# Kernel tuning notes

Measured on AMD Instinct MI355X. Metric: run time of the kernel, lower is better.

## Reference

```python
import jax, jax.numpy as jnp
import numpy as np

N, D, H = 8192, 64, 128
GRID = 256
RADIUS2 = 9  # radius=3 squared


def setup_inputs() -> dict:
    key = jax.random.key(0)
    ks = jax.random.split(key, 9)
    s = lambda k, shape, scale: jax.random.normal(k, shape, dtype=jnp.float32) * scale
    return {
        "positions": jax.random.randint(ks[0], (N, 2), 0, GRID, dtype=jnp.int32),
        "states": s(ks[1], (N, D), 0.1),
        "h": s(ks[2], (N, H), 0.1),
        "c": s(ks[3], (N, H), 0.1),
        "W_ih": s(ks[4], (4 * H, 2 * D), 1.0 / np.sqrt(2 * D)),
        "W_hh": s(ks[5], (4 * H, H), 1.0 / np.sqrt(H)),
        "b": s(ks[6], (4 * H,), 0.01),
        "W_out": s(ks[7], (H, D), 1.0 / np.sqrt(H)),
        "W_role": s(ks[8], (H, 3), 1.0 / np.sqrt(H)),
    }


def reference(positions, states, h, c, W_ih, W_hh, b, W_out, W_role):
    # --- neighbor gather: all-pairs distance on integer grid, radius 3 ---
    d = positions[:, None, :] - positions[None, :, :]          # [N,N,2]
    dist2 = jnp.sum(d * d, axis=-1)                            # [N,N] int32
    mask = (dist2 <= RADIUS2) & (~jnp.eye(N, dtype=bool))      # exclude self
    maskf = mask.astype(states.dtype)
    cnt = jnp.sum(maskf, axis=1, keepdims=True)                # [N,1]
    # mean of neighbor states; zeros when no neighbors (matches zeros fallback)
    nbr_mean = (maskf @ states) / jnp.maximum(cnt, 1.0)        # [N,D]

    # --- per-cell LSTM memory update ---
    x = jnp.concatenate([states, nbr_mean], axis=-1)           # [N,2D]
    gates = x @ W_ih.T + h @ W_hh.T + b                        # [N,4H]
    i_g, f_g, g_g, o_g = jnp.split(gates, 4, axis=-1)
    c_new = jax.nn.sigmoid(f_g) * c + jax.nn.sigmoid(i_g) * jnp.tanh(g_g)
    h_new = jax.nn.sigmoid(o_g) * jnp.tanh(c_new)              # [N,H]

    new_states = h_new @ W_out                                 # [N,D]
    role_probs = jax.nn.softmax(h_new @ W_role, axis=-1)       # [N,3]
    return new_states, role_probs
```

## Files before the change

### kernel.cpp

```cpp
#include <hip/hip_runtime.h>
#include <hip/hip_bf16.h>
#include <math.h>

#define N_CELLS 8192
#define D_DIM 64
#define H_DIM 128
#define GRID_SZ 256
#define NBINS (GRID_SZ * GRID_SZ)
#define BUCKET_CAP 16

typedef short bf16x8 __attribute__((ext_vector_type(8)));
typedef float f32x4 __attribute__((ext_vector_type(4)));

static __device__ __forceinline__ short f2bf(float x) {
    __hip_bfloat16 b = __float2bfloat16(x);
    return __builtin_bit_cast(short, b);
}

__global__ __launch_bounds__(256) void prep(const float* __restrict__ Wih,
                                            const float* __restrict__ Whh,
                                            __hip_bfloat16* __restrict__ Wb,
                                            int4* __restrict__ counts4) {
    int tid = threadIdx.x, b = blockIdx.x;
    if (b >= 128) {
        counts4[(b - 128) * 256 + tid] = make_int4(0, 0, 0, 0);
        return;
    }
    int idx4 = b * 256 + tid;
    int gp = idx4 >> 6, k4 = (idx4 & 63) << 2;
    int group = gp >> 6, c6 = gp & 63, gate = c6 >> 4, hl = c6 & 15;
    int orig = gate * 128 + group * 16 + hl;
    float4 v = (k4 < 128) ? *(const float4*)(Wih + orig * 128 + k4)
                          : *(const float4*)(Whh + orig * 128 + (k4 - 128));
    short4 o = make_short4(f2bf(v.x), f2bf(v.y), f2bf(v.z), f2bf(v.w));
    *(short4*)((short*)Wb + gp * 256 + k4) = o;
}

__global__ __launch_bounds__(256) void bin_fill(const int* __restrict__ positions,
                                                int* __restrict__ counts,
                                                int* __restrict__ buckets) {
    int i = blockIdx.x * 256 + threadIdx.x;
    if (i >= N_CELLS) return;
    int p0 = positions[2 * i], p1 = positions[2 * i + 1];
    int bin = p0 * GRID_SZ + p1;
    int slot = atomicAdd(&counts[bin], 1);
    if (slot < BUCKET_CAP) buckets[bin * BUCKET_CAP + slot] = i;
}

__global__ __launch_bounds__(256) void build_xh(const int* __restrict__ positions,
                                                const float* __restrict__ states,
                                                const float* __restrict__ h,
                                                const int* __restrict__ counts,
                                                const int* __restrict__ buckets,
                                                __hip_bfloat16* __restrict__ xh) {
    int wave = threadIdx.x >> 6;
    int lane = threadIdx.x & 63;
    int i = blockIdx.x * 4 + wave;
    int p0 = positions[2 * i], p1 = positions[2 * i + 1];

    int t = lane;
    int da, db;
    if (t == 0)      { da = -3; db = 0; }
    else if (t < 6)  { da = -2; db = t - 3; }
    else if (t < 11) { da = -1; db = t - 8; }
    else if (t < 18) { da = 0;  db = t - 14; }
    else if (t < 23) { da = 1;  db = t - 20; }
    else if (t < 28) { da = 2;  db = t - 25; }
    else             { da = 3;  db = 0; }

    int q0 = p0 + da, q1 = p1 + db;
    bool ok = (lane < 29) && ((unsigned)q0 < GRID_SZ) && ((unsigned)q1 < GRID_SZ);
    int bin = q0 * GRID_SZ + q1;

    int cl = 0;
    int4 jv = make_int4(0, 0, 0, 0);
    if (ok) {
        cl = counts[bin];
        jv = *(const int4*)(buckets + bin * BUCKET_CAP);
        if (cl > BUCKET_CAP) cl = BUCKET_CAP;
    }

    unsigned long long act = __ballot(cl > 0);
    float acc = 0.0f;
    int cnt = 0;
    while (act) {
        int tb = __ffsll(act) - 1;
        act &= act - 1;
        int ct = __shfl(cl, tb);
        int j0 = __shfl(jv.x, tb), j1 = __shfl(jv.y, tb);
        int j2 = __shfl(jv.z, tb), j3 = __shfl(jv.w, tb);
        if (j0 != i)           { cnt++; acc += states[j0 * D_DIM + lane]; }
        if (ct > 1 && j1 != i) { cnt++; acc += states[j1 * D_DIM + lane]; }
        if (ct > 2 && j2 != i) { cnt++; acc += states[j2 * D_DIM + lane]; }
        if (ct > 3 && j3 != i) { cnt++; acc += states[j3 * D_DIM + lane]; }
        if (ct > 4) {
            int bb = __shfl(bin, tb) * BUCKET_CAP;
            for (int s = 4; s < ct; ++s) {
                int j = buckets[bb + s];
                if (j != i) { cnt++; acc += states[j * D_DIM + lane]; }
            }
        }
    }
    float nbr = (cnt > 0) ? acc / (float)cnt : 0.0f;

    __hip_bfloat16* row = xh + (size_t)i * 256;
    row[lane]       = __float2bfloat16(states[i * D_DIM + lane]);
    row[64 + lane]  = __float2bfloat16(nbr);
    row[128 + lane] = __float2bfloat16(h[i * H_DIM + lane]);
    row[192 + lane] = __float2bfloat16(h[i * H_DIM + 64 + lane]);
}

__global__ __launch_bounds__(512) void mega(const __hip_bfloat16* __restrict__ xh,
                                            const __hip_bfloat16* __restrict__ Wb,
                                            const float* __restrict__ bias,
                                            const float* __restrict__ c_in,
                                            const float* __restrict__ W_out,
                                            const float* __restrict__ W_role,
                                            float* __restrict__ out) {
    __shared__ char smem[69632];
    char* As = smem;
    char* Bs = smem + 4096;
    char* Hl   = smem;
    char* Wohi = smem + 8192;
    char* Wolo = smem + 24576;
    char* Wr   = smem + 40960;

    const int tid  = threadIdx.x;
    const int lane = tid & 63;
    const int wid  = tid >> 6;
    const int wrow = wid >> 2, wcol = wid & 3;
    const int n0 = blockIdx.x * 32;

    const char* aG = (const char*)xh;
    const char* bG = (const char*)Wb;

    f32x4 acc[8] = {};

    for (int kc = 0; kc < 4; ++kc) {
        if (kc) __syncthreads();
        if (tid < 256) {
            int row = tid >> 3, slot = (tid & 7) << 4;
            __builtin_amdgcn_global_load_lds(
                (const __attribute__((address_space(1))) void*)(aG + (size_t)(n0 + row) * 512 + kc * 128 + (slot ^ ((row & 7) << 4))),
                (__attribute__((address_space(3))) void*)(As + row * 128 + slot), 16, 0, 0);
        }
        #pragma unroll
        for (int e = 0; e < 8; ++e) {
            int u = e * 512 + tid;
            int row = u >> 3, slot = (u & 7) << 4;
            __builtin_amdgcn_global_load_lds(
                (const __attribute__((address_space(1))) void*)(bG + (size_t)row * 512 + kc * 128 + (slot ^ ((row & 7) << 4))),
                (__attribute__((address_space(3))) void*)(Bs + row * 128 + slot), 16, 0, 0);
        }
        __syncthreads();

        #pragma unroll
        for (int ks = 0; ks < 2; ++ks) {
            int kb = ks * 64 + ((lane >> 4) << 4);
            int arow = wrow * 16 + (lane & 15);
            bf16x8 av = *(const bf16x8*)(As + arow * 128 + (kb ^ ((arow & 7) << 4)));
            #pragma unroll
            for (int ni = 0; ni < 8; ++ni) {
                int brow = wcol * 128 + ni * 16 + (lane & 15);
                bf16x8 bv = *(const bf16x8*)(Bs + brow * 128 + (kb ^ ((brow & 7) << 4)));
                acc[ni] = __builtin_amdgcn_mfma_f32_16x16x32_bf16(av, bv, acc[ni], 0, 0, 0);
            }
        }
    }
    __syncthreads();

    #pragma unroll
    for (int e = 0; e < 16; ++e) {
        int u = e * 512 + tid;
        int hh = u >> 6, d = u & 63;
        float w = W_out[u];
        float whi = __bfloat162float(__float2bfloat16(w));
        int off = d * 256 + ((hh * 2) ^ ((d & 7) << 4));
        *(short*)(Wohi + off) = f2bf(whi);
        *(short*)(Wolo + off) = f2bf(w - whi);
    }
    #pragma unroll
    for (int e = 0; e < 4; ++e) {
        int u = e * 512 + tid;
        int r = u >> 7, hh = u & 127;
        float w = (r < 3) ? W_role[hh * 3 + r] : 0.0f;
        *(short*)(Wr + r * 256 + ((hh * 2) ^ ((r & 7) << 4))) = f2bf(w);
    }

    #pragma unroll
    for (int b = 0; b < 2; ++b) {
        int hg = (2 * wcol + b) * 16 + (lane & 15);
        float bi = bias[hg], bff = bias[128 + hg], bgg = bias[256 + hg], boo = bias[384 + hg];
        #pragma unroll
        for (int r = 0; r < 4; ++r) {
            int ml = wrow * 16 + ((lane >> 4) << 2) + r;
            float ig = acc[b * 4 + 0][r] + bi;
            float fg = acc[b * 4 + 1][r] + bff;
            float gg = acc[b * 4 + 2][r] + bgg;
            float og = acc[b * 4 + 3][r] + boo;
            float cv = c_in[(size_t)(n0 + ml) * H_DIM + hg];
            float si = 1.0f / (1.0f + expf(-ig));
            float sf = 1.0f / (1.0f + expf(-fg));
            float so = 1.0f / (1.0f + expf(-og));
            float hn = so * tanhf(sf * cv + si * tanhf(gg));
            *(short*)(Hl + ml * 256 + ((hg * 2) ^ ((ml & 7) << 4))) = f2bf(hn);
        }
    }
    __syncthreads();

    const int rb = wid >> 2, db = wid & 3;
    f32x4 oacc = {};
    f32x4 racc = {};
    #pragma unroll
    for (int ks = 0; ks < 4; ++ks) {
        int kb = ks * 64 + ((lane >> 4) << 4);
        int hrow = rb * 16 + (lane & 15);
        bf16x8 hv = *(const bf16x8*)(Hl + hrow * 256 + (kb ^ ((hrow & 7) << 4)));
        int drow = db * 16 + (lane & 15);
        int woff = drow * 256 + (kb ^ ((drow & 7) << 4));
        bf16x8 whi = *(const bf16x8*)(Wohi + woff);
        bf16x8 wlo = *(const bf16x8*)(Wolo + woff);
        oacc = __builtin_amdgcn_mfma_f32_16x16x32_bf16(hv, whi, oacc, 0, 0, 0);
        oacc = __builtin_amdgcn_mfma_f32_16x16x32_bf16(hv, wlo, oacc, 0, 0, 0);
        if (db == 3) {
            int rrow = lane & 15;
            bf16x8 wr = *(const bf16x8*)(Wr + rrow * 256 + (kb ^ ((rrow & 7) << 4)));
            racc = __builtin_amdgcn_mfma_f32_16x16x32_bf16(wr, hv, racc, 0, 0, 0);
        }
    }
    #pragma unroll
    for (int r = 0; r < 4; ++r) {
        int m = n0 + rb * 16 + ((lane >> 4) << 2) + r;
        out[(size_t)m * D_DIM + db * 16 + (lane & 15)] = oacc[r];
    }
    if (db == 3 && lane < 16) {
        int m = n0 + rb * 16 + lane;
        float l0 = racc[0], l1 = racc[1], l2 = racc[2];
        float mx = fmaxf(l0, fmaxf(l1, l2));
        float e0 = expf(l0 - mx), e1 = expf(l1 - mx), e2 = expf(l2 - mx);
        float s = e0 + e1 + e2;
        float* ro = out + (size_t)N_CELLS * D_DIM + (size_t)m * 3;
        ro[0] = e0 / s; ro[1] = e1 / s; ro[2] = e2 / s;
    }
}

extern "C" void kernel_launch(void* const* d_in, const int* in_sizes, int n_in,
                              void* d_out, int out_size, void* d_ws, size_t ws_size,
                              hipStream_t stream) {
    const int*   positions = (const int*)d_in[0];
    const float* states    = (const float*)d_in[1];
    const float* h         = (const float*)d_in[2];
    const float* c         = (const float*)d_in[3];
    const float* Wih       = (const float*)d_in[4];
    const float* Whh       = (const float*)d_in[5];
    const float* bias      = (const float*)d_in[6];
    const float* Wout      = (const float*)d_in[7];
    const float* Wrole     = (const float*)d_in[8];
    float* out             = (float*)d_out;

    char* ws = (char*)d_ws;
    int*            counts  = (int*)ws;
    int*            buckets = (int*)(ws + 262144);
    __hip_bfloat16* xh      = (__hip_bfloat16*)(ws + 4456448);
    __hip_bfloat16* Wb      = (__hip_bfloat16*)(ws + 8650752);

    prep<<<192, 256, 0, stream>>>(Wih, Whh, Wb, (int4*)counts);
    bin_fill<<<N_CELLS / 256, 256, 0, stream>>>(positions, counts, buckets);
    build_xh<<<N_CELLS / 4, 256, 0, stream>>>(positions, states, h, counts, buckets, xh);
    mega<<<N_CELLS / 32, 512, 0, stream>>>(xh, Wb, bias, c, Wout, Wrole, out);
}
```

Before: 34.59 us.

## Precompute output/role weight bf16 splits in prep and async-load them into LDS

Moves the W_out hi/lo bf16 split and the W_role conversion out of each mega block and into the prep kernel, which writes them to workspace. Mega then loads them into dedicated LDS regions with async global_load_lds at the start, overlapping that load with the gate GEMM. It also prefetches the c values into registers before the GEMM. The cost is LDS growing from 68KB to 112KB per block, which may limit occupancy, plus a larger prep launch.

Measured after the change: 33.61 us. -2.8%, faster.

```diff
diff --git a/kernel.cpp b/kernel.cpp
--- a/kernel.cpp
+++ b/kernel.cpp
@@ -19,21 +19,41 @@
 
 __global__ __launch_bounds__(256) void prep(const float* __restrict__ Wih,
                                             const float* __restrict__ Whh,
+                                            const float* __restrict__ W_out,
+                                            const float* __restrict__ W_role,
                                             __hip_bfloat16* __restrict__ Wb,
+                                            __hip_bfloat16* __restrict__ Wohi,
+                                            __hip_bfloat16* __restrict__ Wolo,
+                                            __hip_bfloat16* __restrict__ Wr,
                                             int4* __restrict__ counts4) {
     int tid = threadIdx.x, b = blockIdx.x;
-    if (b >= 128) {
+    if (b < 128) {
+        int idx4 = b * 256 + tid;
+        int gp = idx4 >> 6, k4 = (idx4 & 63) << 2;
+        int group = gp >> 6, c6 = gp & 63, gate = c6 >> 4, hl = c6 & 15;
+        int orig = gate * 128 + group * 16 + hl;
+        float4 v = (k4 < 128) ? *(const float4*)(Wih + orig * 128 + k4)
+                              : *(const float4*)(Whh + orig * 128 + (k4 - 128));
+        short4 o = make_short4(f2bf(v.x), f2bf(v.y), f2bf(v.z), f2bf(v.w));
+        *(short4*)((short*)Wb + gp * 256 + k4) = o;
+    } else if (b < 192) {
         counts4[(b - 128) * 256 + tid] = make_int4(0, 0, 0, 0);
-        return;
-    }
-    int idx4 = b * 256 + tid;
-    int gp = idx4 >> 6, k4 = (idx4 & 63) << 2;
-    int group = gp >> 6, c6 = gp & 63, gate = c6 >> 4, hl = c6 & 15;
-    int orig = gate * 128 + group * 16 + hl;
-    float4 v = (k4 < 128) ? *(const float4*)(Wih + orig * 128 + k4)
-                          : *(const float4*)(Whh + orig * 128 + (k4 - 128));
-    short4 o = make_short4(f2bf(v.x), f2bf(v.y), f2bf(v.z), f2bf(v.w));
-    *(short4*)((short*)Wb + gp * 256 + k4) = o;
+    } else if (b < 224) {
+        int u = (b - 192) * 256 + tid;
+        int hh = u >> 6, d = u & 63;
+        float w = W_out[u];
+        float whi = __bfloat162float(__float2bfloat16(w));
+        Wohi[d * 128 + hh] = __float2bfloat16(whi);
+        Wolo[d * 128 + hh] = __float2bfloat16(w - whi);
+    } else {
+        #pragma unroll
+        for (int e = 0; e < 8; ++e) {
+            int u = e * 256 + tid;
+            int r = u >> 7, hh = u & 127;
+            float w = (r < 3) ? W_role[hh * 3 + r] : 0.0f;
+            Wr[r * 128 + hh] = __float2bfloat16(w);
+        }
+    }
 }
 
 __global__ __launch_bounds__(256) void bin_fill(const int* __restrict__ positions,
@@ -114,22 +134,56 @@
                                             const __hip_bfloat16* __restrict__ Wb,
                                             const float* __restrict__ bias,
                                             const float* __restrict__ c_in,
-                                            const float* __restrict__ W_out,
-                                            const float* __restrict__ W_role,
+                                            const __hip_bfloat16* __restrict__ Wohi,
+                                            const __hip_bfloat16* __restrict__ Wolo,
+                                            const __hip_bfloat16* __restrict__ Wr,
                                             float* __restrict__ out) {
-    __shared__ char smem[69632];
-    char* As = smem;
-    char* Bs = smem + 4096;
-    char* Hl   = smem;
-    char* Wohi = smem + 8192;
-    char* Wolo = smem + 24576;
-    char* Wr   = smem + 40960;
+    __shared__ char smem[114688];
+    char* As  = smem;
+    char* Bs  = smem + 4096;
+    char* Whi = smem + 69632;
+    char* Wlo = smem + 86016;
+    char* Wrl = smem + 102400;
+    char* Hl  = smem + 106496;
 
     const int tid  = threadIdx.x;
     const int lane = tid & 63;
     const int wid  = tid >> 6;
     const int wrow = wid >> 2, wcol = wid & 3;
     const int n0 = blockIdx.x * 32;
+
+    const char* hiG = (const char*)Wohi;
+    const char* loG = (const char*)Wolo;
+    const char* wrG = (const char*)Wr;
+    #pragma unroll
+    for (int e = 0; e < 2; ++e) {
+        int u = e * 512 + tid;
+        int row = u >> 4, slot = (u & 15) << 4;
+        int src = row * 256 + (slot ^ ((row & 7) << 4));
+        __builtin_amdgcn_global_load_lds(
+            (const __attribute__((address_space(1))) void*)(hiG + src),
+            (__attribute__((address_space(3))) void*)(Whi + row * 256 + slot), 16, 0, 0);
+        __builtin_amdgcn_global_load_lds(
+            (const __attribute__((address_space(1))) void*)(loG + src),
+            (__attribute__((address_space(3))) void*)(Wlo + row * 256 + slot), 16, 0, 0);
+    }
+    if (tid < 256) {
+        int row = tid >> 4, slot = (tid & 15) << 4;
+        __builtin_amdgcn_global_load_lds(
+            (const __attribute__((address_space(1))) void*)(wrG + row * 256 + (slot ^ ((row & 7) << 4))),
+            (__attribute__((address_space(3))) void*)(Wrl + row * 256 + slot), 16, 0, 0);
+    }
+
+    float cv[2][4];
+    #pragma unroll
+    for (int b = 0; b < 2; ++b) {
+        int hg = (2 * wcol + b) * 16 + (lane & 15);
+        #pragma unroll
+        for (int r = 0; r < 4; ++r) {
+            int ml = wrow * 16 + ((lane >> 4) << 2) + r;
+            cv[b][r] = c_in[(size_t)(n0 + ml) * H_DIM + hg];
+        }
+    }
 
     const char* aG = (const char*)xh;
     const char* bG = (const char*)Wb;
@@ -167,25 +221,6 @@
             }
         }
     }
-    __syncthreads();
-
-    #pragma unroll
-    for (int e = 0; e < 16; ++e) {
-        int u = e * 512 + tid;
-        int hh = u >> 6, d = u & 63;
-        float w = W_out[u];
-        float whi = __bfloat162float(__float2bfloat16(w));
-        int off = d * 256 + ((hh * 2) ^ ((d & 7) << 4));
-        *(short*)(Wohi + off) = f2bf(whi);
-        *(short*)(Wolo + off) = f2bf(w - whi);
-    }
-    #pragma unroll
-    for (int e = 0; e < 4; ++e) {
-        int u = e * 512 + tid;
-        int r = u >> 7, hh = u & 127;
-        float w = (r < 3) ? W_role[hh * 3 + r] : 0.0f;
-        *(short*)(Wr + r * 256 + ((hh * 2) ^ ((r & 7) << 4))) = f2bf(w);
-    }
 
     #pragma unroll
     for (int b = 0; b < 2; ++b) {
@@ -198,11 +233,10 @@
             float fg = acc[b * 4 + 1][r] + bff;
             float gg = acc[b * 4 + 2][r] + bgg;
             float og = acc[b * 4 + 3][r] + boo;
-            float cv = c_in[(size_t)(n0 + ml) * H_DIM + hg];
             float si = 1.0f / (1.0f + expf(-ig));
             float sf = 1.0f / (1.0f + expf(-fg));
             float so = 1.0f / (1.0f + expf(-og));
-            float hn = so * tanhf(sf * cv + si * tanhf(gg));
+            float hn = so * tanhf(sf * cv[b][r] + si * tanhf(gg));
             *(short*)(Hl + ml * 256 + ((hg * 2) ^ ((ml & 7) << 4))) = f2bf(hn);
         }
     }
@@ -218,13 +252,13 @@
         bf16x8 hv = *(const bf16x8*)(Hl + hrow * 256 + (kb ^ ((hrow & 7) << 4)));
         int drow = db * 16 + (lane & 15);
         int woff = drow * 256 + (kb ^ ((drow & 7) << 4));
-        bf16x8 whi = *(const bf16x8*)(Wohi + woff);
-        bf16x8 wlo = *(const bf16x8*)(Wolo + woff);
+        bf16x8 whi = *(const bf16x8*)(Whi + woff);
+        bf16x8 wlo = *(const bf16x8*)(Wlo + woff);
         oacc = __builtin_amdgcn_mfma_f32_16x16x32_bf16(hv, whi, oacc, 0, 0, 0);
         oacc = __builtin_amdgcn_mfma_f32_16x16x32_bf16(hv, wlo, oacc, 0, 0, 0);
         if (db == 3) {
             int rrow = lane & 15;
-            bf16x8 wr = *(const bf16x8*)(Wr + rrow * 256 + (kb ^ ((rrow & 7) << 4)));
+            bf16x8 wr = *(const bf16x8*)(Wrl + rrow * 256 + (kb ^ ((rrow & 7) << 4)));
             racc = __builtin_amdgcn_mfma_f32_16x16x32_bf16(wr, hv, racc, 0, 0, 0);
         }
     }
@@ -263,9 +297,12 @@
     int*            buckets = (int*)(ws + 262144);
     __hip_bfloat16* xh      = (__hip_bfloat16*)(ws + 4456448);
     __hip_bfloat16* Wb      = (__hip_bfloat16*)(ws + 8650752);
-
-    prep<<<192, 256, 0, stream>>>(Wih, Whh, Wb, (int4*)counts);
+    __hip_bfloat16* Wohi    = (__hip_bfloat16*)(ws + 8912896);
+    __hip_bfloat16* Wolo    = (__hip_bfloat16*)(ws + 8929280);
+    __hip_bfloat16* Wr      = (__hip_bfloat16*)(ws + 8945664);
+
+    prep<<<225, 256, 0, stream>>>(Wih, Whh, Wout, Wrole, Wb, Wohi, Wolo, Wr, (int4*)counts);
     bin_fill<<<N_CELLS / 256, 256, 0, stream>>>(positions, counts, buckets);
     build_xh<<<N_CELLS / 4, 256, 0, stream>>>(positions, states, h, counts, buckets, xh);
-    mega<<<N_CELLS / 32, 512, 0, stream>>>(xh, Wb, bias, c, Wout, Wrole, out);
-}
+    mega<<<N_CELLS / 32, 512, 0, stream>>>(xh, Wb, bias, c, Wohi, Wolo, Wr, out);
+}
```
